# Kernel optimization log

Measured on AMD Instinct MI355X. Metric: run time of the kernel, lower is better.

## Reference

```python
import jax, jax.numpy as jnp
import numpy as np

WINDOW = 5       # window_size (<= input_length)
OUT_LEN = 96     # output_length


def setup_inputs() -> dict:
    key = jax.random.key(0)
    # x: [batch, input_length, input_dim]
    x = jax.random.normal(key, (2048, 512, 64), dtype=jnp.float32)
    return {"x": x}


def reference(x):
    # Carry only the last WINDOW rows of the (growing) history: [B, W, D].
    carry0 = x[:, -WINDOW:, :]

    def step(carry, _):
        f = jnp.mean(carry, axis=1)  # [B, D] forecast = mean of last WINDOW rows
        carry = jnp.concatenate([carry[:, 1:, :], f[:, None, :]], axis=1)
        return carry, f

    _, preds = jax.lax.scan(step, carry0, None, length=OUT_LEN)  # [T, B, D]
    return jnp.transpose(preds, (1, 0, 2))  # [B, output_length, D]
```

## Files before the change

### kernel.cpp

```cpp
#include <hip/hip_runtime.h>


#define SMA_B 2048
#define SMA_S 512
#define SMA_C 64
#define SMA_W 5
#define SMA_T 96

__global__ __launch_bounds__(256) void StatisticalSMA_kernel(
    const float* __restrict__ x, float* __restrict__ out) {
    int tid = blockIdx.x * blockDim.x + threadIdx.x;
    int b = tid >> 6;
    int c = tid & 63;

    const float* xp = x + (size_t)b * (SMA_S * SMA_C) + (SMA_S - SMA_W) * SMA_C + c;
    float w0 = xp[0 * SMA_C];
    float w1 = xp[1 * SMA_C];
    float w2 = xp[2 * SMA_C];
    float w3 = xp[3 * SMA_C];
    float w4 = xp[4 * SMA_C];

    float* op = out + (size_t)b * (SMA_T * SMA_C) + c;
    #pragma unroll
    for (int t = 0; t < SMA_T; ++t) {
        float f = (w0 + w1 + w2 + w3 + w4) * 0.2f;
        op[t * SMA_C] = f;
        w0 = w1; w1 = w2; w2 = w3; w3 = w4; w4 = f;
    }
}

extern "C" void kernel_launch(void* const* d_in, const int* in_sizes, int n_in,
                              void* d_out, int out_size, void* d_ws, size_t ws_size,
                              hipStream_t stream) {
    const float* x = (const float*)d_in[0];
    float* out = (float*)d_out;
    const int total = SMA_B * SMA_C;
    const int block = 256;
    const int grid = total / block;
    StatisticalSMA_kernel<<<grid, block, 0, stream>>>(x, out);
}
```

Baseline: 14.47 us.

## Replace sequential SMA recurrence with precomputed linear coefficients split across time

Each forecast step is written as a fixed linear combination of the five initial window rows, with the coefficients computed at compile time into a constant-memory table. This removes the serial 96-step dependency chain, so each block handles one batch row and four wavefronts each produce 24 output steps in parallel. The grid grows from 512 to 2048 blocks, and each thread now issues only 24 dependent-free stores. In exchange every wavefront reloads the same window values, and rounding differs slightly from the sequential float recurrence.

```diff
diff --git a/kernel.cpp b/kernel.cpp
--- a/kernel.cpp
+++ b/kernel.cpp
@@ -6,26 +6,51 @@
 #define SMA_C 64
 #define SMA_W 5
 #define SMA_T 96
+#define TPG   24
+
+struct CoefTable { float c[SMA_T][SMA_W]; };
+
+constexpr CoefTable make_table() {
+    CoefTable t{};
+    double w[SMA_W][SMA_W] = {};
+    for (int i = 0; i < SMA_W; ++i) w[i][i] = 1.0;
+    for (int s = 0; s < SMA_T; ++s) {
+        double f[SMA_W];
+        for (int j = 0; j < SMA_W; ++j) {
+            double acc = 0.0;
+            for (int i = 0; i < SMA_W; ++i) acc += w[i][j];
+            f[j] = acc * 0.2;
+        }
+        for (int j = 0; j < SMA_W; ++j) t.c[s][j] = (float)f[j];
+        for (int i = 0; i < SMA_W - 1; ++i)
+            for (int j = 0; j < SMA_W; ++j) w[i][j] = w[i + 1][j];
+        for (int j = 0; j < SMA_W; ++j) w[SMA_W - 1][j] = f[j];
+    }
+    return t;
+}
+
+constexpr CoefTable kCoef = make_table();
+__constant__ CoefTable COEF = kCoef;
 
 __global__ __launch_bounds__(256) void StatisticalSMA_kernel(
     const float* __restrict__ x, float* __restrict__ out) {
-    int tid = blockIdx.x * blockDim.x + threadIdx.x;
-    int b = tid >> 6;
-    int c = tid & 63;
+    const int b  = blockIdx.x;
+    const int c  = threadIdx.x & 63;
+    const int wg = threadIdx.x >> 6;
 
     const float* xp = x + (size_t)b * (SMA_S * SMA_C) + (SMA_S - SMA_W) * SMA_C + c;
-    float w0 = xp[0 * SMA_C];
-    float w1 = xp[1 * SMA_C];
-    float w2 = xp[2 * SMA_C];
-    float w3 = xp[3 * SMA_C];
-    float w4 = xp[4 * SMA_C];
+    const float w0 = xp[0 * SMA_C];
+    const float w1 = xp[1 * SMA_C];
+    const float w2 = xp[2 * SMA_C];
+    const float w3 = xp[3 * SMA_C];
+    const float w4 = xp[4 * SMA_C];
 
-    float* op = out + (size_t)b * (SMA_T * SMA_C) + c;
+    float* op = out + (size_t)b * (SMA_T * SMA_C) + (size_t)(wg * TPG) * SMA_C + c;
     #pragma unroll
-    for (int t = 0; t < SMA_T; ++t) {
-        float f = (w0 + w1 + w2 + w3 + w4) * 0.2f;
-        op[t * SMA_C] = f;
-        w0 = w1; w1 = w2; w2 = w3; w3 = w4; w4 = f;
+    for (int tt = 0; tt < TPG; ++tt) {
+        const float* cf = COEF.c[wg * TPG + tt];
+        float f = w0 * cf[0] + w1 * cf[1] + w2 * cf[2] + w3 * cf[3] + w4 * cf[4];
+        op[tt * SMA_C] = f;
     }
 }
 
@@ -34,8 +59,5 @@
                               hipStream_t stream) {
     const float* x = (const float*)d_in[0];
     float* out = (float*)d_out;
-    const int total = SMA_B * SMA_C;
-    const int block = 256;
-    const int grid = total / block;
-    StatisticalSMA_kernel<<<grid, block, 0, stream>>>(x, out);
+    StatisticalSMA_kernel<<<SMA_B, 256, 0, stream>>>(x, out);
 }
```

Result: slower. 18.43 us (+27.4%).

## Split forecast horizon into chunks via precomputed linear window jumps, vectorize

Applied to the files above, without the earlier changes.

The SMA recurrence is linear, so compile-time coefficient matrices let each of four wavefronts jump straight to the window state at the start of its 24-step chunk instead of running the serial recurrence from step zero. Each thread now handles four channels with float4 loads and stores, and each wavefront covers four batches. This shortens the per-thread serial dependency chain and widens memory accesses. The cost is that every wavefront reloads the same input window, and the jumped coefficients change the float rounding slightly compared with step-by-step evaluation.

```diff
diff --git a/kernel.cpp b/kernel.cpp
--- a/kernel.cpp
+++ b/kernel.cpp
@@ -6,26 +6,91 @@
 #define SMA_C 64
 #define SMA_W 5
 #define SMA_T 96
+#define NCHUNK 4
+#define TPC 24
+
+struct ChunkWin { float c[NCHUNK][SMA_W][SMA_W]; };
+
+constexpr ChunkWin make_cw() {
+    ChunkWin out{};
+    double w[SMA_W][SMA_W] = {};
+    for (int i = 0; i < SMA_W; ++i) w[i][i] = 1.0;
+    for (int q = 0; q < NCHUNK; ++q) {
+        for (int i = 0; i < SMA_W; ++i)
+            for (int j = 0; j < SMA_W; ++j) out.c[q][i][j] = (float)w[i][j];
+        for (int s = 0; s < TPC; ++s) {
+            double f[SMA_W];
+            for (int j = 0; j < SMA_W; ++j) {
+                double a = 0.0;
+                for (int i = 0; i < SMA_W; ++i) a += w[i][j];
+                f[j] = a * 0.2;
+            }
+            for (int i = 0; i + 1 < SMA_W; ++i)
+                for (int j = 0; j < SMA_W; ++j) w[i][j] = w[i + 1][j];
+            for (int j = 0; j < SMA_W; ++j) w[SMA_W - 1][j] = f[j];
+        }
+    }
+    return out;
+}
+constexpr ChunkWin kCW = make_cw();
+
+template <int Q>
+__device__ __forceinline__ void run_chunk(const float4 (&w)[SMA_W],
+                                          float* __restrict__ op) {
+    float4 v[SMA_W];
+    #pragma unroll
+    for (int i = 0; i < SMA_W; ++i) {
+        float ax = 0.f, ay = 0.f, az = 0.f, aw = 0.f;
+        bool first = true;
+        #pragma unroll
+        for (int j = 0; j < SMA_W; ++j) {
+            const float cj = kCW.c[Q][i][j];
+            if (cj == 0.0f) continue;
+            if (first) {
+                ax = cj * w[j].x; ay = cj * w[j].y;
+                az = cj * w[j].z; aw = cj * w[j].w;
+                first = false;
+            } else {
+                ax += cj * w[j].x; ay += cj * w[j].y;
+                az += cj * w[j].z; aw += cj * w[j].w;
+            }
+        }
+        v[i] = make_float4(ax, ay, az, aw);
+    }
+    #pragma unroll
+    for (int t = 0; t < TPC; ++t) {
+        float4 f;
+        f.x = (v[0].x + v[1].x + v[2].x + v[3].x + v[4].x) * 0.2f;
+        f.y = (v[0].y + v[1].y + v[2].y + v[3].y + v[4].y) * 0.2f;
+        f.z = (v[0].z + v[1].z + v[2].z + v[3].z + v[4].z) * 0.2f;
+        f.w = (v[0].w + v[1].w + v[2].w + v[3].w + v[4].w) * 0.2f;
+        *reinterpret_cast<float4*>(op + t * SMA_C) = f;
+        v[0] = v[1]; v[1] = v[2]; v[2] = v[3]; v[3] = v[4]; v[4] = f;
+    }
+}
 
 __global__ __launch_bounds__(256) void StatisticalSMA_kernel(
     const float* __restrict__ x, float* __restrict__ out) {
-    int tid = blockIdx.x * blockDim.x + threadIdx.x;
-    int b = tid >> 6;
-    int c = tid & 63;
+    const int lane = threadIdx.x & 63;
+    const int q    = __builtin_amdgcn_readfirstlane((int)(threadIdx.x >> 6));
+    const int colg = lane & 15;
+    const int bsub = lane >> 4;
+    const int b    = blockIdx.x * 4 + bsub;
 
-    const float* xp = x + (size_t)b * (SMA_S * SMA_C) + (SMA_S - SMA_W) * SMA_C + c;
-    float w0 = xp[0 * SMA_C];
-    float w1 = xp[1 * SMA_C];
-    float w2 = xp[2 * SMA_C];
-    float w3 = xp[3 * SMA_C];
-    float w4 = xp[4 * SMA_C];
+    const float* xp = x + (size_t)b * (SMA_S * SMA_C)
+                        + (SMA_S - SMA_W) * SMA_C + colg * 4;
+    float4 w[SMA_W];
+    #pragma unroll
+    for (int i = 0; i < SMA_W; ++i)
+        w[i] = *reinterpret_cast<const float4*>(xp + i * SMA_C);
 
-    float* op = out + (size_t)b * (SMA_T * SMA_C) + c;
-    #pragma unroll
-    for (int t = 0; t < SMA_T; ++t) {
-        float f = (w0 + w1 + w2 + w3 + w4) * 0.2f;
-        op[t * SMA_C] = f;
-        w0 = w1; w1 = w2; w2 = w3; w3 = w4; w4 = f;
+    float* op = out + (size_t)b * (SMA_T * SMA_C)
+                    + (size_t)(q * TPC) * SMA_C + colg * 4;
+    switch (q) {
+        case 0: run_chunk<0>(w, op); break;
+        case 1: run_chunk<1>(w, op); break;
+        case 2: run_chunk<2>(w, op); break;
+        default: run_chunk<3>(w, op); break;
     }
 }
 
@@ -34,8 +99,5 @@
                               hipStream_t stream) {
     const float* x = (const float*)d_in[0];
     float* out = (float*)d_out;
-    const int total = SMA_B * SMA_C;
-    const int block = 256;
-    const int grid = total / block;
-    StatisticalSMA_kernel<<<grid, block, 0, stream>>>(x, out);
+    StatisticalSMA_kernel<<<SMA_B / 4, 256, 0, stream>>>(x, out);
 }
```

After: 14.44 us. Within noise of the previous version (-0.2%).
